# Kernel tuning notes

Hardware: AMD Instinct MI355X
Metric: run time of the kernel (lower is better)

The kernel has to match this reference:

```python
import jax, jax.numpy as jnp
import numpy as np

B, T, D, H, FC = 32768, 7, 40, 64, 32


def lstm_layer(x_seq, W_ih, W_hh, b_ih, b_hh):
    # x_seq: [T, B, Din]; weights in PyTorch layout: W_ih [4H, Din], W_hh [4H, H]
    # Precompute the input contribution to all gates outside the scan.
    gx_seq = jnp.einsum('tbd,gd->tbg', x_seq, W_ih) + b_ih + b_hh  # [T, B, 4H]
    h0 = jnp.zeros((x_seq.shape[1], W_hh.shape[1]), x_seq.dtype)
    c0 = jnp.zeros_like(h0)

    def step(carry, gx):
        h, c = carry
        g = gx + h @ W_hh.T                      # [B, 4H]
        i, f, gg, o = jnp.split(g, 4, axis=-1)   # PyTorch gate order: i, f, g, o
        i = jax.nn.sigmoid(i)
        f = jax.nn.sigmoid(f)
        gg = jnp.tanh(gg)
        o = jax.nn.sigmoid(o)
        c = f * c + i * gg
        h = o * jnp.tanh(c)
        return (h, c), h

    (_, _), hs = jax.lax.scan(step, (h0, c0), gx_seq)
    return hs  # [T, B, H]


def setup_inputs() -> dict:
    key = jax.random.key(0)
    ks = jax.random.split(key, 13)
    s_in = 1.0 / np.sqrt(H)
    u = lambda k, shape: jax.random.uniform(k, shape, jnp.float32, -s_in, s_in)
    return {
        'x': jax.random.normal(ks[0], (B, T, D), jnp.float32),
        'W_ih0': u(ks[1], (4 * H, D)),
        'W_hh0': u(ks[2], (4 * H, H)),
        'b_ih0': u(ks[3], (4 * H,)),
        'b_hh0': u(ks[4], (4 * H,)),
        'W_ih1': u(ks[5], (4 * H, H)),
        'W_hh1': u(ks[6], (4 * H, H)),
        'b_ih1': u(ks[7], (4 * H,)),
        'b_hh1': u(ks[8], (4 * H,)),
        'W1': u(ks[9], (FC, H)),
        'b1': u(ks[10], (FC,)),
        'W2': u(ks[11], (1, FC)),
        'b2': u(ks[12], (1,)),
    }


def reference(x, W_ih0, W_hh0, b_ih0, b_hh0, W_ih1, W_hh1, b_ih1, b_hh1, W1, b1, W2, b2):
    xs = jnp.transpose(x, (1, 0, 2))                    # [T, B, D]
    h1 = lstm_layer(xs, W_ih0, W_hh0, b_ih0, b_hh0)     # [T, B, H]
    h2 = lstm_layer(h1, W_ih1, W_hh1, b_ih1, b_hh1)     # [T, B, H]
    last = h2[-1]                                       # out[:, -1, :] -> [B, H]
    # dropout is identity in eval mode
    hid = jax.nn.relu(last @ W1.T + b1)                 # [B, 32]
    return hid @ W2.T + b2                              # [B, 1]
```

## Files before the change

### kernel.cpp

```cpp
#include <hip/hip_runtime.h>

#define TT 7
#define DD 40
#define HH 64
#define RB 64
#define NRT 4
#define NTH 512
#define HS 72
#define XP 44
#define L2E 1.44269504088896340736f

typedef _Float16 f16x8 __attribute__((ext_vector_type(8)));
typedef float f32x4 __attribute__((ext_vector_type(4)));

#define MFMA(acc, a, b) acc = __builtin_amdgcn_mfma_f32_16x16x32_f16(a, b, acc, 0, 0, 0)

__device__ __forceinline__ float fast_rcp(float x) { return __builtin_amdgcn_rcpf(x); }
__device__ __forceinline__ float ex2(float x) { return __builtin_amdgcn_exp2f(x); }

typedef __attribute__((address_space(3))) unsigned lds_u32_t;
typedef const __attribute__((address_space(1))) unsigned glb_u32_t;
__device__ __forceinline__ void gl_lds16(const void* g, void* l) {
  __builtin_amdgcn_global_load_lds((glb_u32_t*)g, (lds_u32_t*)l, 16, 0, 0);
}

__device__ __forceinline__ f16x8 zf() {
  f16x8 r;
  #pragma unroll
  for (int i = 0; i < 8; ++i) r[i] = (_Float16)0.f;
  return r;
}
__device__ __forceinline__ f16x8 cvt8s(const float* p, float s) {
  float4 a = *(const float4*)p, b = *(const float4*)(p + 4);
  f16x8 r;
  r[0] = (_Float16)(a.x * s); r[1] = (_Float16)(a.y * s);
  r[2] = (_Float16)(a.z * s); r[3] = (_Float16)(a.w * s);
  r[4] = (_Float16)(b.x * s); r[5] = (_Float16)(b.y * s);
  r[6] = (_Float16)(b.z * s); r[7] = (_Float16)(b.w * s);
  return r;
}
__device__ __forceinline__ f16x8 cvt8(const float* p) {
  float4 a = *(const float4*)p, b = *(const float4*)(p + 4);
  f16x8 r;
  r[0] = (_Float16)a.x; r[1] = (_Float16)a.y; r[2] = (_Float16)a.z; r[3] = (_Float16)a.w;
  r[4] = (_Float16)b.x; r[5] = (_Float16)b.y; r[6] = (_Float16)b.z; r[7] = (_Float16)b.w;
  return r;
}
__device__ __forceinline__ f16x8 pk8(float4 a, float4 b) {
  f16x8 r;
  auto p0 = __builtin_amdgcn_cvt_pkrtz(a.x, a.y);
  auto p1 = __builtin_amdgcn_cvt_pkrtz(a.z, a.w);
  auto p2 = __builtin_amdgcn_cvt_pkrtz(b.x, b.y);
  auto p3 = __builtin_amdgcn_cvt_pkrtz(b.z, b.w);
  r[0] = p0[0]; r[1] = p0[1]; r[2] = p1[0]; r[3] = p1[1];
  r[4] = p2[0]; r[5] = p2[1]; r[6] = p3[0]; r[7] = p3[1];
  return r;
}

__global__ __launch_bounds__(NTH, 2) void lstm2_ls3_kernel(
    const float* __restrict__ x,
    const float* __restrict__ Wih0, const float* __restrict__ Whh0,
    const float* __restrict__ bih0, const float* __restrict__ bhh0,
    const float* __restrict__ Wih1, const float* __restrict__ Whh1,
    const float* __restrict__ bih1, const float* __restrict__ bhh1,
    const float* __restrict__ W1, const float* __restrict__ b1,
    const float* __restrict__ W2, const float* __restrict__ b2,
    float* __restrict__ out)
{
  __shared__ __align__(16) unsigned short s_h[4][RB * HS];
  __shared__ __align__(16) float s_x[2][RB * XP];
  __shared__ __align__(16) float s_fc[2112];

  const int tid = threadIdx.x;
  const int l   = tid & 63;
  const int wv  = tid >> 6;
  const bool L0 = (wv < 4);
  const int wn  = wv & 3;
  const int l15 = l & 15;
  const int lg  = l >> 4;
  const int jj  = wn * 16 + l15;
  const int k0l = lg * 8;
  const int blk = blockIdx.x;
  const float* xg = x + (size_t)blk * RB * (TT * DD);

  const int c0 = tid, c1 = 512 + tid;
  const int r0 = c0 / 11, p0 = c0 - r0 * 11;
  const int r1 = c1 / 11, p1 = c1 - r1 * 11;
  const bool v0 = (p0 < 10);
  const bool v1 = (c1 < 704) && (p1 < 10);
  const float* xs0 = xg + r0 * (TT * DD) + p0 * 4;
  const float* xs1 = xg + r1 * (TT * DD) + p1 * 4;
  const int d0 = wv * 256, d1 = 2048 + wv * 256;

  if (v0) gl_lds16(xs0, &s_x[0][d0]);
  if (v1) gl_lds16(xs1, &s_x[0][d1]);
  gl_lds16(W1 + tid * 4, &s_fc[wv * 256]);
  if (tid < 16) {
    const float* src = (tid < 8) ? (b1 + tid * 4) : (W2 + (tid - 8) * 4);
    gl_lds16(src, &s_fc[2048]);
  }

  f16x8 W[16];
  float biasv[4];
  if (L0) {
    #pragma unroll
    for (int g = 0; g < 4; ++g) {
      const float gs = (g == 2) ? 2.f * L2E : L2E;
      int n = g * 64 + jj;
      W[g]      = cvt8s(&Wih0[n * DD + k0l], gs);
      W[4 + g]  = (lg == 0) ? cvt8s(&Wih0[n * DD + 32], gs) : zf();
      W[8 + g]  = cvt8s(&Whh0[n * HH + k0l], gs);
      W[12 + g] = cvt8s(&Whh0[n * HH + 32 + k0l], gs);
      biasv[g] = (bih0[n] + bhh0[n]) * gs;
    }
  } else {
    #pragma unroll
    for (int g = 0; g < 4; ++g) {
      const float gs = (g == 2) ? 2.f * L2E : L2E;
      int n = g * 64 + jj;
      W[g]      = cvt8s(&Wih1[n * HH + k0l], gs);
      W[4 + g]  = cvt8s(&Wih1[n * HH + 32 + k0l], gs);
      W[8 + g]  = cvt8s(&Whh1[n * HH + k0l], gs);
      W[12 + g] = cvt8s(&Whh1[n * HH + 32 + k0l], gs);
      biasv[g] = (bih1[n] + bhh1[n]) * gs;
    }
  }

  float cst[NRT][4];
  #pragma unroll
  for (int rt = 0; rt < NRT; ++rt)
    #pragma unroll
    for (int r = 0; r < 4; ++r) cst[rt][r] = 0.f;

  __syncthreads();

  #pragma unroll 1
  for (int s = 0; s < TT; ++s) {
    if (s) __syncthreads();
    if (s < TT - 1) {
      float* xd = &s_x[(s + 1) & 1][0];
      const int so = (s + 1) * DD;
      if (v0) gl_lds16(xs0 + so, xd + d0);
      if (v1) gl_lds16(xs1 + so, xd + d1);
    }
    const int p1r = (s - 1) & 1;

    if (L0) {
      const float* xb = &s_x[s & 1][0];
      #pragma unroll
      for (int rt = 0; rt < NRT; ++rt) {
        const float* xr = xb + (rt * 16 + l15) * XP;
        f16x8 xh = pk8(*(const float4*)(xr + k0l), *(const float4*)(xr + k0l + 4));
        f16x8 xm = xh;
        if (lg == 0) xm = pk8(*(const float4*)(xr + 32), *(const float4*)(xr + 36));

        f32x4 acc[4];
        #pragma unroll
        for (int g = 0; g < 4; ++g)
          acc[g] = (f32x4){biasv[g], biasv[g], biasv[g], biasv[g]};

        __builtin_amdgcn_s_setprio(1);
        #pragma unroll
        for (int g = 0; g < 4; ++g) MFMA(acc[g], xh, W[g]);
        #pragma unroll
        for (int g = 0; g < 4; ++g) MFMA(acc[g], xm, W[4 + g]);
        if (s) {
          const unsigned short* hp = &s_h[p1r][(rt * 16 + l15) * HS + k0l];
          f16x8 h1a = *(const f16x8*)hp;
          f16x8 h1b = *(const f16x8*)(hp + 32);
          #pragma unroll
          for (int g = 0; g < 4; ++g) MFMA(acc[g], h1a, W[8 + g]);
          #pragma unroll
          for (int g = 0; g < 4; ++g) MFMA(acc[g], h1b, W[12 + g]);
        }
        __builtin_amdgcn_s_setprio(0);

        #pragma unroll
        for (int r = 0; r < 4; ++r) {
          float ig = fast_rcp(1.f + ex2(-acc[0][r]));
          float fg = fast_rcp(1.f + ex2(-acc[1][r]));
          float gg = 1.f - 2.f * fast_rcp(1.f + ex2(acc[2][r]));
          float og = fast_rcp(1.f + ex2(-acc[3][r]));
          float c  = fg * cst[rt][r] + ig * gg;
          cst[rt][r] = c;
          float h  = og * (1.f - 2.f * fast_rcp(1.f + ex2(c * (2.f * L2E))));
          s_h[s & 1][(rt * 16 + lg * 4 + r) * HS + jj] =
              __builtin_bit_cast(unsigned short, (_Float16)h);
        }
      }
    } else if (s) {
      #pragma unroll
      for (int rt = 0; rt < NRT; ++rt) {
        const unsigned short* hp = &s_h[p1r][(rt * 16 + l15) * HS + k0l];
        f16x8 h1a = *(const f16x8*)hp;
        f16x8 h1b = *(const f16x8*)(hp + 32);

        f32x4 acc[4];
        #pragma unroll
        for (int g = 0; g < 4; ++g)
          acc[g] = (f32x4){biasv[g], biasv[g], biasv[g], biasv[g]};

        __builtin_amdgcn_s_setprio(1);
        #pragma unroll
        for (int g = 0; g < 4; ++g) MFMA(acc[g], h1a, W[g]);
        #pragma unroll
        for (int g = 0; g < 4; ++g) MFMA(acc[g], h1b, W[4 + g]);
        if (s >= 2) {
          const unsigned short* qp = &s_h[2 + (s & 1)][(rt * 16 + l15) * HS + k0l];
          f16x8 q0 = *(const f16x8*)qp;
          f16x8 q1 = *(const f16x8*)(qp + 32);
          #pragma unroll
          for (int g = 0; g < 4; ++g) MFMA(acc[g], q0, W[8 + g]);
          #pragma unroll
          for (int g = 0; g < 4; ++g) MFMA(acc[g], q1, W[12 + g]);
        }
        __builtin_amdgcn_s_setprio(0);

        #pragma unroll
        for (int r = 0; r < 4; ++r) {
          float ig = fast_rcp(1.f + ex2(-acc[0][r]));
          float fg = fast_rcp(1.f + ex2(-acc[1][r]));
          float gg = 1.f - 2.f * fast_rcp(1.f + ex2(acc[2][r]));
          float og = fast_rcp(1.f + ex2(-acc[3][r]));
          float c  = fg * cst[rt][r] + ig * gg;
          cst[rt][r] = c;
          float h  = og * (1.f - 2.f * fast_rcp(1.f + ex2(c * (2.f * L2E))));
          s_h[2 + p1r][(rt * 16 + lg * 4 + r) * HS + jj] =
              __builtin_bit_cast(unsigned short, (_Float16)h);
        }
      }
    }
  }

  __syncthreads();
  if (!L0) {
    #pragma unroll
    for (int rt = 0; rt < NRT; ++rt) {
      const unsigned short* hp = &s_h[0][(rt * 16 + l15) * HS + k0l];
      f16x8 h1a = *(const f16x8*)hp;
      f16x8 h1b = *(const f16x8*)(hp + 32);
      const unsigned short* qp = &s_h[3][(rt * 16 + l15) * HS + k0l];
      f16x8 q0 = *(const f16x8*)qp;
      f16x8 q1 = *(const f16x8*)(qp + 32);
      f32x4 acc[4];
      #pragma unroll
      for (int g = 0; g < 4; ++g)
        acc[g] = (f32x4){biasv[g], biasv[g], biasv[g], biasv[g]};
      __builtin_amdgcn_s_setprio(1);
      #pragma unroll
      for (int g = 0; g < 4; ++g) MFMA(acc[g], h1a, W[g]);
      #pragma unroll
      for (int g = 0; g < 4; ++g) MFMA(acc[g], h1b, W[4 + g]);
      #pragma unroll
      for (int g = 0; g < 4; ++g) MFMA(acc[g], q0, W[8 + g]);
      #pragma unroll
      for (int g = 0; g < 4; ++g) MFMA(acc[g], q1, W[12 + g]);
      __builtin_amdgcn_s_setprio(0);
      #pragma unroll
      for (int r = 0; r < 4; ++r) {
        float ig = fast_rcp(1.f + ex2(-acc[0][r]));
        float fg = fast_rcp(1.f + ex2(-acc[1][r]));
        float gg = 1.f - 2.f * fast_rcp(1.f + ex2(acc[2][r]));
        float og = fast_rcp(1.f + ex2(-acc[3][r]));
        float c  = fg * cst[rt][r] + ig * gg;
        float h  = og * (1.f - 2.f * fast_rcp(1.f + ex2(c * (2.f * L2E))));
        s_h[1][(rt * 16 + lg * 4 + r) * HS + jj] =
            __builtin_bit_cast(unsigned short, (_Float16)h);
      }
    }
  }
  __syncthreads();

  {
    const int twv = wv >> 1;
    const int fh  = wv & 1;
    const unsigned short* ap = &s_h[1][(twv * 16 + l15) * HS + k0l];
    f16x8 A0 = *(const f16x8*)ap;
    f16x8 A1 = *(const f16x8*)(ap + 32);
    int n = fh * 16 + l15;
    f16x8 Bf0 = cvt8(&s_fc[n * 64 + k0l]);
    f16x8 Bf1 = cvt8(&s_fc[n * 64 + 32 + k0l]);
    float bb = s_fc[2048 + n];
    f32x4 accf = (f32x4){bb, bb, bb, bb};
    MFMA(accf, A0, Bf0);
    MFMA(accf, A1, Bf1);
    float* hid = &s_x[0][0];
    #pragma unroll
    for (int r = 0; r < 4; ++r)
      hid[(twv * 16 + lg * 4 + r) * 36 + fh * 16 + l15] = fmaxf(accf[r], 0.f);
  }
  __syncthreads();
  if (tid < RB) {
    const float* hid = &s_x[0][0];
    float a = b2[0];
    #pragma unroll
    for (int kq = 0; kq < 8; ++kq) {
      float4 hv = *(const float4*)&hid[tid * 36 + kq * 4];
      float4 wv4 = *(const float4*)&s_fc[2080 + kq * 4];
      a += hv.x * wv4.x + hv.y * wv4.y + hv.z * wv4.z + hv.w * wv4.w;
    }
    out[blk * RB + tid] = a;
  }
}

extern "C" void kernel_launch(void* const* d_in, const int* in_sizes, int n_in,
                              void* d_out, int out_size, void* d_ws, size_t ws_size,
                              hipStream_t stream) {
  const float* x    = (const float*)d_in[0];
  const float* Wih0 = (const float*)d_in[1];
  const float* Whh0 = (const float*)d_in[2];
  const float* bih0 = (const float*)d_in[3];
  const float* bhh0 = (const float*)d_in[4];
  const float* Wih1 = (const float*)d_in[5];
  const float* Whh1 = (const float*)d_in[6];
  const float* bih1 = (const float*)d_in[7];
  const float* bhh1 = (const float*)d_in[8];
  const float* W1   = (const float*)d_in[9];
  const float* b1   = (const float*)d_in[10];
  const float* W2   = (const float*)d_in[11];
  const float* b2   = (const float*)d_in[12];
  float* out = (float*)d_out;

  const int Btot = in_sizes[0] / (TT * DD);
  dim3 grid(Btot / RB), block(NTH);
  lstm2_ls3_kernel<<<grid, block, 0, stream>>>(
      x, Wih0, Whh0, bih0, bhh0, Wih1, Whh1, bih1, bhh1, W1, b1, W2, b2, out);
}
```

Measured before the change: 67.07 us.

## Prefetch x two steps ahead and pre-convert to fp16 in LDS

Input tiles are now fetched two timesteps ahead into the float staging buffers. All 512 threads cooperatively convert the next step's tile to packed fp16 in a new LDS buffer, so the layer-0 waves read fp16 fragments directly instead of converting floats inside the critical MFMA loop. Launch bounds are raised from 2 to 4 blocks per CU, which tightens the register budget and risks spilling the 16 weight fragments. The conversion adds LDS traffic and work for the layer-1 waves.

```diff
diff --git a/kernel.cpp b/kernel.cpp
--- a/kernel.cpp
+++ b/kernel.cpp
@@ -8,6 +8,7 @@
 #define NTH 512
 #define HS 72
 #define XP 44
+#define XH 40
 #define L2E 1.44269504088896340736f
 
 typedef _Float16 f16x8 __attribute__((ext_vector_type(8)));
@@ -46,18 +47,8 @@
   r[4] = (_Float16)b.x; r[5] = (_Float16)b.y; r[6] = (_Float16)b.z; r[7] = (_Float16)b.w;
   return r;
 }
-__device__ __forceinline__ f16x8 pk8(float4 a, float4 b) {
-  f16x8 r;
-  auto p0 = __builtin_amdgcn_cvt_pkrtz(a.x, a.y);
-  auto p1 = __builtin_amdgcn_cvt_pkrtz(a.z, a.w);
-  auto p2 = __builtin_amdgcn_cvt_pkrtz(b.x, b.y);
-  auto p3 = __builtin_amdgcn_cvt_pkrtz(b.z, b.w);
-  r[0] = p0[0]; r[1] = p0[1]; r[2] = p1[0]; r[3] = p1[1];
-  r[4] = p2[0]; r[5] = p2[1]; r[6] = p3[0]; r[7] = p3[1];
-  return r;
-}
-
-__global__ __launch_bounds__(NTH, 2) void lstm2_ls3_kernel(
+
+__global__ __launch_bounds__(NTH, 4) void lstm2_ls5_kernel(
     const float* __restrict__ x,
     const float* __restrict__ Wih0, const float* __restrict__ Whh0,
     const float* __restrict__ bih0, const float* __restrict__ bhh0,
@@ -69,16 +60,16 @@
 {
   __shared__ __align__(16) unsigned short s_h[4][RB * HS];
   __shared__ __align__(16) float s_x[2][RB * XP];
+  __shared__ __align__(16) unsigned short s_xh[2][RB * XH];
   __shared__ __align__(16) float s_fc[2112];
 
   const int tid = threadIdx.x;
   const int l   = tid & 63;
   const int wv  = tid >> 6;
   const bool L0 = (wv < 4);
-  const int wn  = wv & 3;
   const int l15 = l & 15;
   const int lg  = l >> 4;
-  const int jj  = wn * 16 + l15;
+  const int jj  = (wv & 3) * 16 + l15;
   const int k0l = lg * 8;
   const int blk = blockIdx.x;
   const float* xg = x + (size_t)blk * RB * (TT * DD);
@@ -94,7 +85,9 @@
 
   if (v0) gl_lds16(xs0, &s_x[0][d0]);
   if (v1) gl_lds16(xs1, &s_x[0][d1]);
-  gl_lds16(W1 + tid * 4, &s_fc[wv * 256]);
+  if (v0) gl_lds16(xs0 + DD, &s_x[1][d0]);
+  if (v1) gl_lds16(xs1 + DD, &s_x[1][d1]);
+  gl_lds16(W1 + tid * 4, &s_fc[d0]);
   if (tid < 16) {
     const float* src = (tid < 8) ? (b1 + tid * 4) : (W2 + (tid - 8) * 4);
     gl_lds16(src, &s_fc[2048]);
@@ -134,25 +127,53 @@
 
   __syncthreads();
 
+  {
+    const float* src = &s_x[0][0];
+    unsigned* dst = (unsigned*)&s_xh[0][0];
+    #pragma unroll
+    for (int it = 0; it < 3; ++it) {
+      int i = it * NTH + tid;
+      if (i < RB * 20) {
+        int row = i / 20, c2 = i - row * 20;
+        float2 f = *(const float2*)&src[row * XP + c2 * 2];
+        auto p = __builtin_amdgcn_cvt_pkrtz(f.x, f.y);
+        dst[row * 20 + c2] = __builtin_bit_cast(unsigned, p);
+      }
+    }
+  }
+  __syncthreads();
+
   #pragma unroll 1
   for (int s = 0; s < TT; ++s) {
     if (s) __syncthreads();
+    if (s < TT - 2) {
+      const int so = (s + 2) * DD;
+      if (v0) gl_lds16(xs0 + so, &s_x[s & 1][d0]);
+      if (v1) gl_lds16(xs1 + so, &s_x[s & 1][d1]);
+    }
     if (s < TT - 1) {
-      float* xd = &s_x[(s + 1) & 1][0];
-      const int so = (s + 1) * DD;
-      if (v0) gl_lds16(xs0 + so, xd + d0);
-      if (v1) gl_lds16(xs1 + so, xd + d1);
+      const float* src = &s_x[(s + 1) & 1][0];
+      unsigned* dst = (unsigned*)&s_xh[(s + 1) & 1][0];
+      #pragma unroll
+      for (int it = 0; it < 3; ++it) {
+        int i = it * NTH + tid;
+        if (i < RB * 20) {
+          int row = i / 20, c2 = i - row * 20;
+          float2 f = *(const float2*)&src[row * XP + c2 * 2];
+          auto p = __builtin_amdgcn_cvt_pkrtz(f.x, f.y);
+          dst[row * 20 + c2] = __builtin_bit_cast(unsigned, p);
+        }
+      }
     }
     const int p1r = (s - 1) & 1;
 
     if (L0) {
-      const float* xb = &s_x[s & 1][0];
+      const unsigned short* xb = &s_xh[s & 1][0];
       #pragma unroll
       for (int rt = 0; rt < NRT; ++rt) {
-        const float* xr = xb + (rt * 16 + l15) * XP;
-        f16x8 xh = pk8(*(const float4*)(xr + k0l), *(const float4*)(xr + k0l + 4));
-        f16x8 xm = xh;
-        if (lg == 0) xm = pk8(*(const float4*)(xr + 32), *(const float4*)(xr + 36));
+        const unsigned short* xr = xb + (rt * 16 + l15) * XH;
+        f16x8 xh = *(const f16x8*)(xr + k0l);
+        f16x8 xm = *(const f16x8*)(xr + ((lg == 0) ? 32 : 0));
 
         f32x4 acc[4];
         #pragma unroll
@@ -323,6 +344,6 @@
 
   const int Btot = in_sizes[0] / (TT * DD);
   dim3 grid(Btot / RB), block(NTH);
-  lstm2_ls3_kernel<<<grid, block, 0, stream>>>(
+  lstm2_ls5_kernel<<<grid, block, 0, stream>>>(
       x, Wih0, Whh0, bih0, bhh0, Wih1, Whh1, bih1, bhh1, W1, b1, W2, b2, out);
 }
```

Measured after the change: 73.71 us. +9.9%, slower.
